# Kernel tuning notes

Hardware: AMD Instinct MI355X
Metric: run time of the kernel (lower is better)

The kernel has to match this reference:

```python
import jax, jax.numpy as jnp
import numpy as np

N_SIN = 3  # fcn_n_sin (static)


def setup_inputs() -> dict:
    key = jax.random.key(0)
    ks = jax.random.split(key, 5)
    B, I, O, H = 256, 128, 128, 32
    F = 1 + 2 * N_SIN
    return {
        "x": jax.random.normal(ks[0], (B, I), dtype=jnp.float32),
        "W1": jax.random.normal(ks[1], (I, O, H, F), dtype=jnp.float32) * 0.3,
        "W2": jax.random.normal(ks[2], (I, O, 1, H), dtype=jnp.float32) * 0.3,
        "B1": jax.random.normal(ks[3], (I, O, H), dtype=jnp.float32) * 0.1,
        "B2": jax.random.normal(ks[4], (I, O, 1), dtype=jnp.float32) * 0.1,
    }


def reference(x, W1, W2, B1, B2):
    # x: [B, I]; per-(i,o) edge MLP on a scalar input, summed over i.
    omega = (2.0 ** jnp.arange(N_SIN)).astype(x.dtype)          # [S]
    ox = x[..., None] * omega                                    # [B, I, S]
    feat = jnp.concatenate([x[..., None], jnp.sin(ox), jnp.cos(ox)], axis=-1)  # [B, I, 1+2S]
    # First linear: per-edge [F -> H]
    h = jnp.einsum('bif,iohf->bioh', feat, W1) + B1              # [B, I, O, H]
    h = jax.nn.silu(h)
    # Second linear: per-edge [H -> 1], then sum over input dims i
    out = jnp.einsum('bioh,ioh->bio', h, W2[:, :, 0, :]) + B2[:, :, 0]  # [B, I, O]
    return out.sum(axis=1)                                       # [B, O]
```

## Files before the change

### kernel.cpp

```cpp
#include <hip/hip_runtime.h>

#define B_DIM 256
#define I_DIM 128
#define O_DIM 128
#define H_DIM 32
#define F_DIM 7
#define ICHUNK 8
#define NCHUNK (I_DIM / ICHUNK)

__global__ __launch_bounds__(256, 4)
void fcnkan_kernel(const float* __restrict__ x,
                   const float* __restrict__ W1,
                   const float* __restrict__ W2,
                   const float* __restrict__ B1,
                   const float* __restrict__ B2,
                   float* __restrict__ out) {
    __shared__ __align__(16) float w1b1[ICHUNK * H_DIM * 8];
    __shared__ float w2s[ICHUNK * H_DIM];
    __shared__ float b2s[ICHUNK];

    const int tid = threadIdx.x;
    const int o   = blockIdx.x;
    const int ic0 = blockIdx.y * ICHUNK;

    for (int e = tid; e < ICHUNK * H_DIM * F_DIM; e += 256) {
        int il = e / (H_DIM * F_DIM);
        int r  = e - il * (H_DIM * F_DIM);
        int h  = r / F_DIM;
        int f  = r - h * F_DIM;
        w1b1[(il * H_DIM + h) * 8 + f] =
            W1[(size_t)((ic0 + il) * O_DIM + o) * (H_DIM * F_DIM) + r];
    }
    for (int e = tid; e < ICHUNK * H_DIM; e += 256) {
        int il = e >> 5, h = e & 31;
        int io = (ic0 + il) * O_DIM + o;
        w1b1[(il * H_DIM + h) * 8 + 7] = B1[io * H_DIM + h];
        w2s[e]                         = W2[io * H_DIM + h];
    }
    if (tid < ICHUNK) b2s[tid] = B2[(ic0 + tid) * O_DIM + o];

    const float4* xp = reinterpret_cast<const float4*>(x + (size_t)tid * I_DIM + ic0);
    float4 x0 = xp[0], x1 = xp[1];
    float xr[8] = {x0.x, x0.y, x0.z, x0.w, x1.x, x1.y, x1.z, x1.w};

    __syncthreads();

    float acc = 0.f;

    #pragma unroll
    for (int il = 0; il < ICHUNK; ++il) {
        float xv = xr[il];
        float s1 = __sinf(xv), c1 = __cosf(xv);
        float s2 = 2.f * s1 * c1, c2 = 1.f - 2.f * s1 * s1;
        float s4 = 2.f * s2 * c2, c4 = 1.f - 2.f * s2 * s2;

        const float4* wrow  = reinterpret_cast<const float4*>(w1b1 + il * H_DIM * 8);
        const float*  w2row = w2s + il * H_DIM;

        #pragma unroll 4
        for (int h = 0; h < H_DIM; ++h) {
            float4 wa = wrow[h * 2];
            float4 wb = wrow[h * 2 + 1];
            float z = fmaf(wa.x, xv, wb.w);
            z = fmaf(wa.y, s1, z);
            z = fmaf(wa.z, s2, z);
            z = fmaf(wa.w, s4, z);
            z = fmaf(wb.x, c1, z);
            z = fmaf(wb.y, c2, z);
            z = fmaf(wb.z, c4, z);
            float sg = __builtin_amdgcn_rcpf(1.f + __expf(-z));
            acc = fmaf(z * sg, w2row[h], acc);
        }
    }

    float b2c = 0.f;
    #pragma unroll
    for (int il = 0; il < ICHUNK; ++il) b2c += b2s[il];

    atomicAdd(&out[(size_t)tid * O_DIM + o], acc + b2c);
}

extern "C" void kernel_launch(void* const* d_in, const int* in_sizes, int n_in,
                              void* d_out, int out_size, void* d_ws, size_t ws_size,
                              hipStream_t stream) {
    const float* x  = (const float*)d_in[0];
    const float* W1 = (const float*)d_in[1];
    const float* W2 = (const float*)d_in[2];
    const float* B1 = (const float*)d_in[3];
    const float* B2 = (const float*)d_in[4];
    float* out = (float*)d_out;

    hipMemsetAsync(out, 0, (size_t)out_size * sizeof(float), stream);
    dim3 grid(O_DIM, NCHUNK);
    fcnkan_kernel<<<grid, 256, 0, stream>>>(x, W1, W2, B1, B2, out);
}
```

Before: 126.3 us.

## Compute first edge-MLP layer with bf16 MFMA instead of scalar FMAs

Moves the per-edge F->H projection onto MFMA 16x16x32 bf16 instructions. Features and W1 are packed into bf16 fragments padded with zeros, and B1 is folded in as the accumulator init. SiLU and W2 stay on the vector ALU, followed by a cross-lane shuffle reduction over the hidden dimension. The input chunk per block doubles and the shared-memory staging is dropped in favour of direct global loads. This uses only 7 of 32 K slots, so most of the MFMA work is wasted, and it adds bf16 rounding error on x, the sin/cos features and W1.

```diff
diff --git a/kernel.cpp b/kernel.cpp
--- a/kernel.cpp
+++ b/kernel.cpp
@@ -1,83 +1,118 @@
 #include <hip/hip_runtime.h>
+#include <hip/hip_bf16.h>
 
 #define B_DIM 256
 #define I_DIM 128
 #define O_DIM 128
 #define H_DIM 32
 #define F_DIM 7
-#define ICHUNK 8
+#define ICHUNK 16
 #define NCHUNK (I_DIM / ICHUNK)
 
-__global__ __launch_bounds__(256, 4)
-void fcnkan_kernel(const float* __restrict__ x,
-                   const float* __restrict__ W1,
-                   const float* __restrict__ W2,
-                   const float* __restrict__ B1,
-                   const float* __restrict__ B2,
-                   float* __restrict__ out) {
-    __shared__ __align__(16) float w1b1[ICHUNK * H_DIM * 8];
-    __shared__ float w2s[ICHUNK * H_DIM];
-    __shared__ float b2s[ICHUNK];
+typedef __attribute__((ext_vector_type(8))) short short8;
+typedef __attribute__((ext_vector_type(4))) float float4v;
 
-    const int tid = threadIdx.x;
-    const int o   = blockIdx.x;
-    const int ic0 = blockIdx.y * ICHUNK;
+__device__ inline short bf16s(float v) {
+    union { __hip_bfloat16 h; short s; } u;
+    u.h = __float2bfloat16(v);
+    return u.s;
+}
 
-    for (int e = tid; e < ICHUNK * H_DIM * F_DIM; e += 256) {
-        int il = e / (H_DIM * F_DIM);
-        int r  = e - il * (H_DIM * F_DIM);
-        int h  = r / F_DIM;
-        int f  = r - h * F_DIM;
-        w1b1[(il * H_DIM + h) * 8 + f] =
-            W1[(size_t)((ic0 + il) * O_DIM + o) * (H_DIM * F_DIM) + r];
-    }
-    for (int e = tid; e < ICHUNK * H_DIM; e += 256) {
-        int il = e >> 5, h = e & 31;
-        int io = (ic0 + il) * O_DIM + o;
-        w1b1[(il * H_DIM + h) * 8 + 7] = B1[io * H_DIM + h];
-        w2s[e]                         = W2[io * H_DIM + h];
-    }
-    if (tid < ICHUNK) b2s[tid] = B2[(ic0 + tid) * O_DIM + o];
+__global__ __launch_bounds__(256, 2)
+void fcnkan_mfma(const float* __restrict__ x,
+                 const float* __restrict__ W1,
+                 const float* __restrict__ W2,
+                 const float* __restrict__ B1,
+                 const float* __restrict__ B2,
+                 float* __restrict__ out) {
+    const int tid  = threadIdx.x;
+    const int o    = blockIdx.x;
+    const int ic0  = blockIdx.y * ICHUNK;
+    const int w    = tid >> 6;
+    const int lane = tid & 63;
+    const int m    = lane & 15;
+    const int q    = lane >> 4;
 
-    const float4* xp = reinterpret_cast<const float4*>(x + (size_t)tid * I_DIM + ic0);
-    float4 x0 = xp[0], x1 = xp[1];
-    float xr[8] = {x0.x, x0.y, x0.z, x0.w, x1.x, x1.y, x1.z, x1.w};
+    const short8 zero8 = {};
 
-    __syncthreads();
+    float b2c = 0.f;
+    for (int il = 0; il < ICHUNK; ++il) b2c += B2[(size_t)(ic0 + il) * O_DIM + o];
 
-    float acc = 0.f;
+    float acc[16];
+    #pragma unroll
+    for (int r = 0; r < 16; ++r) acc[r] = 0.f;
 
-    #pragma unroll
+    #pragma unroll 1
     for (int il = 0; il < ICHUNK; ++il) {
-        float xv = xr[il];
-        float s1 = __sinf(xv), c1 = __cosf(xv);
-        float s2 = 2.f * s1 * c1, c2 = 1.f - 2.f * s1 * s1;
-        float s4 = 2.f * s2 * c2, c4 = 1.f - 2.f * s2 * s2;
+        const int i = ic0 + il;
 
-        const float4* wrow  = reinterpret_cast<const float4*>(w1b1 + il * H_DIM * 8);
-        const float*  w2row = w2s + il * H_DIM;
+        short8 afrag[4];
+        #pragma unroll
+        for (int t = 0; t < 4; ++t) {
+            float xv = x[(size_t)(w * 64 + t * 16 + m) * I_DIM + i];
+            float s1 = __sinf(xv), c1 = __cosf(xv);
+            float s2 = 2.f * s1 * c1, c2 = 1.f - 2.f * s1 * s1;
+            float s4 = 2.f * s2 * c2, c4 = 1.f - 2.f * s2 * s2;
+            short8 a;
+            a[0] = bf16s(xv); a[1] = bf16s(s1); a[2] = bf16s(s2); a[3] = bf16s(s4);
+            a[4] = bf16s(c1); a[5] = bf16s(c2); a[6] = bf16s(c4); a[7] = 0;
+            afrag[t] = (q == 0) ? a : zero8;
+        }
 
-        #pragma unroll 4
-        for (int h = 0; h < H_DIM; ++h) {
-            float4 wa = wrow[h * 2];
-            float4 wb = wrow[h * 2 + 1];
-            float z = fmaf(wa.x, xv, wb.w);
-            z = fmaf(wa.y, s1, z);
-            z = fmaf(wa.z, s2, z);
-            z = fmaf(wa.w, s4, z);
-            z = fmaf(wb.x, c1, z);
-            z = fmaf(wb.y, c2, z);
-            z = fmaf(wb.z, c4, z);
-            float sg = __builtin_amdgcn_rcpf(1.f + __expf(-z));
-            acc = fmaf(z * sg, w2row[h], acc);
+        const size_t iobase = (size_t)i * O_DIM + o;
+        const size_t w1base = iobase * (H_DIM * F_DIM);
+        short8 bfrag[2];
+        float  b1v[2], w2v[2];
+        #pragma unroll
+        for (int nt = 0; nt < 2; ++nt) {
+            int h = nt * 16 + m;
+            const float* wr = W1 + w1base + (size_t)h * F_DIM;
+            short8 bfr;
+            #pragma unroll
+            for (int f = 0; f < F_DIM; ++f) bfr[f] = bf16s(wr[f]);
+            bfr[7] = 0;
+            bfrag[nt] = (q == 0) ? bfr : zero8;
+            b1v[nt] = B1[iobase * H_DIM + h];
+            w2v[nt] = W2[iobase * H_DIM + h];
+        }
+
+        #pragma unroll
+        for (int nt = 0; nt < 2; ++nt) {
+            float4v c0 = {b1v[nt], b1v[nt], b1v[nt], b1v[nt]};
+            #pragma unroll
+            for (int t = 0; t < 4; ++t) {
+                float4v z = __builtin_amdgcn_mfma_f32_16x16x32_bf16(
+                    afrag[t], bfrag[nt], c0, 0, 0, 0);
+                #pragma unroll
+                for (int r = 0; r < 4; ++r) {
+                    float zz = z[r];
+                    float sg = __builtin_amdgcn_rcpf(1.f + __expf(-zz));
+                    acc[t * 4 + r] = fmaf(zz * sg, w2v[nt], acc[t * 4 + r]);
+                }
+            }
         }
     }
 
-    float b2c = 0.f;
     #pragma unroll
-    for (int il = 0; il < ICHUNK; ++il) b2c += b2s[il];
+    for (int r = 0; r < 16; ++r) {
+        float v = acc[r];
+        v += __shfl_xor(v, 1, 64);
+        v += __shfl_xor(v, 2, 64);
+        v += __shfl_xor(v, 4, 64);
+        v += __shfl_xor(v, 8, 64);
+        acc[r] = v;
+    }
 
-    atomicAdd(&out[(size_t)tid * O_DIM + o], acc + b2c);
+    if (m == 0) {
+        #pragma unroll
+        for (int t = 0; t < 4; ++t) {
+            #pragma unroll
+            for (int r = 0; r < 4; ++r) {
+                int b = w * 64 + t * 16 + q * 4 + r;
+                atomicAdd(&out[(size_t)b * O_DIM + o], acc[t * 4 + r] + b2c);
+            }
+        }
+    }
 }
 
 extern "C" void kernel_launch(void* const* d_in, const int* in_sizes, int n_in,
@@ -92,5 +127,5 @@
 
     hipMemsetAsync(out, 0, (size_t)out_size * sizeof(float), stream);
     dim3 grid(O_DIM, NCHUNK);
-    fcnkan_kernel<<<grid, 256, 0, stream>>>(x, W1, W2, B1, B2, out);
+    fcnkan_mfma<<<grid, 256, 0, stream>>>(x, W1, W2, B1, B2, out);
 }
```

Measured after the change: 123.4 us. 1.02x faster.
